# Kernel tuning notes

Measured on AMD Instinct MI355X. Metric: run time of the kernel, lower is better.

## Reference

```python
import jax, jax.numpy as jnp
import numpy as np

N_HEAD = 16
N_EMBD = 1024
HEAD_DIM = N_EMBD // N_HEAD


def setup_inputs() -> dict:
    key = jax.random.key(0)
    k1, k2, k3 = jax.random.split(key, 3)
    B, T, C = 4, 2048, N_EMBD
    scale = 1.0 / np.sqrt(C)
    x = jax.random.normal(k1, (B, T, C), dtype=jnp.float32)
    W_attn = jax.random.normal(k2, (C, 3 * C), dtype=jnp.float32) * scale
    W_proj = jax.random.normal(k3, (C, C), dtype=jnp.float32) * scale
    return {"x": x, "W_attn": W_attn, "W_proj": W_proj}


def reference(x, W_attn, W_proj):
    B, T, C = x.shape
    H, D = N_HEAD, HEAD_DIM
    qkv = x @ W_attn  # [B,T,3C]
    q, k, v = jnp.split(qkv, 3, axis=-1)
    # [B,H,T,D]
    q = q.reshape(B, T, H, D).transpose(0, 2, 1, 3)
    k = k.reshape(B, T, H, D).transpose(0, 2, 1, 3)
    v = v.reshape(B, T, H, D).transpose(0, 2, 1, 3)
    att = jnp.einsum("bhqd,bhkd->bhqk", q, k) * (1.0 / np.sqrt(D))
    mask = jnp.tril(jnp.ones((T, T), dtype=bool))
    att = jnp.where(mask, att, -jnp.inf)
    att = jax.nn.softmax(att, axis=-1)
    y = jnp.einsum("bhqk,bhkd->bhqd", att, v)
    y = y.transpose(0, 2, 1, 3).reshape(B, T, C)
    return y @ W_proj
```

## Files before the change

### kernel.cpp

```cpp
#include <hip/hip_runtime.h>
#include <hip/hip_bf16.h>

typedef __bf16 bf16x8 __attribute__((ext_vector_type(8)));
typedef __bf16 bf16x4 __attribute__((ext_vector_type(4)));
typedef float  f32x4  __attribute__((ext_vector_type(4)));

#define MFMA16(A, B, C) __builtin_amdgcn_mfma_f32_16x16x32_bf16((A), (B), (C), 0, 0, 0)

static constexpr int TB = 4;
static constexpr int TT = 2048;
static constexpr int TC = 1024;
static constexpr int TH = 16;
static constexpr int TD = 64;
static constexpr int TM = TB * TT;

__device__ __forceinline__ void gload16(const __bf16* g, __bf16* l) {
  __builtin_amdgcn_global_load_lds(
      (const __attribute__((address_space(1))) unsigned int*)g,
      (__attribute__((address_space(3))) unsigned int*)l, 16, 0, 0);
}

__device__ __forceinline__ void transpose_tile(const float* __restrict__ w,
                                               __bf16* __restrict__ wt,
                                               int K, int N, int bx, int by,
                                               __bf16 (*tile)[72], int tid) {
  const int k0 = by * 64, n0 = bx * 64;
#pragma unroll
  for (int it = 0; it < 4; ++it) {
    int c = tid + it * 256;
    int row = c >> 4, cc = (c & 15) * 4;
    float4 v = *(const float4*)(w + (size_t)(k0 + row) * N + n0 + cc);
    tile[row][cc + 0] = (__bf16)v.x;
    tile[row][cc + 1] = (__bf16)v.y;
    tile[row][cc + 2] = (__bf16)v.z;
    tile[row][cc + 3] = (__bf16)v.w;
  }
  __syncthreads();
#pragma unroll
  for (int it = 0; it < 2; ++it) {
    int c = tid + it * 256;
    int n = c >> 3, kk = (c & 7) * 8;
    bf16x8 v;
#pragma unroll
    for (int j = 0; j < 8; ++j) v[j] = tile[kk + j][n];
    *(bf16x8*)(wt + (size_t)(n0 + n) * K + k0 + kk) = v;
  }
}

__global__ __launch_bounds__(256) void k_prep(const float* __restrict__ x,
                                              __bf16* __restrict__ xb,
                                              const float* __restrict__ Wa,
                                              __bf16* __restrict__ wat,
                                              const float* __restrict__ Wp,
                                              __bf16* __restrict__ wpt) {
  __shared__ __align__(16) __bf16 tile[64][72];
  const int bid = blockIdx.x, tid = threadIdx.x;
  if (bid < 2048) {
    const int n4 = (TM * TC) / 4;
    const int stride = 2048 * 256;
    for (int i = bid * 256 + tid; i < n4; i += stride) {
      float4 v = *(const float4*)(x + (size_t)i * 4);
      bf16x4 o;
      o[0] = (__bf16)v.x; o[1] = (__bf16)v.y; o[2] = (__bf16)v.z; o[3] = (__bf16)v.w;
      *(bf16x4*)(xb + (size_t)i * 4) = o;
    }
  } else if (bid < 2816) {
    const int b2 = bid - 2048;
    transpose_tile(Wa, wat, 1024, 3072, b2 % 48, b2 / 48, tile, tid);
  } else {
    const int b2 = bid - 2816;
    transpose_tile(Wp, wpt, 1024, 1024, b2 % 16, b2 / 16, tile, tid);
  }
}

template <int EPI>
__global__ __launch_bounds__(256, 3) void k_gemm(const __bf16* __restrict__ A,
                                                 const __bf16* __restrict__ Bt,
                                                 int N, float* __restrict__ outf,
                                                 __bf16* __restrict__ Qo,
                                                 __bf16* __restrict__ Ko,
                                                 __bf16* __restrict__ Vto) {
  __shared__ __align__(16) __bf16 As[128 * 64];
  __shared__ __align__(16) __bf16 Bs[128 * 64];
  const int gx = gridDim.x;
  const int nwg = gx * gridDim.y;
  int id = blockIdx.y * gx + blockIdx.x;
  id = (id & 7) * (nwg >> 3) + (id >> 3);
  const int bm = id / gx, bn = id % gx;
  const int tid = threadIdx.x, lane = tid & 63, wid = tid >> 6;
  const int wr = wid >> 1, wc = wid & 1;
  const int lr = lane & 15, lg = lane >> 4;

  f32x4 acc[4][4];
  const f32x4 zero = {0.f, 0.f, 0.f, 0.f};
#pragma unroll
  for (int mi = 0; mi < 4; ++mi)
#pragma unroll
    for (int ni = 0; ni < 4; ++ni) acc[mi][ni] = zero;

  const __bf16* Ab = A + (size_t)bm * 128 * 1024;
  const __bf16* Bb = Bt + (size_t)bn * 128 * 1024;

  const int rr = wid * 8 + (lane >> 3);
  const int sc = (lane & 7) ^ (lane >> 3);

  int offA[4][2], offB[4][2];
#pragma unroll
  for (int i = 0; i < 4; ++i)
#pragma unroll
    for (int kk = 0; kk < 2; ++kk) {
      const int xo = ((((kk << 2) + lg) ^ (lr & 7)) << 3);
      offA[i][kk] = (wr * 64 + i * 16 + lr) * 64 + xo;
      offB[i][kk] = (wc * 64 + i * 16 + lr) * 64 + xo;
    }

  for (int k0 = 0; k0 < 1024; k0 += 64) {
#pragma unroll
    for (int it = 0; it < 4; ++it) {
      const int r = it * 32 + rr;
      gload16(Ab + (size_t)r * 1024 + k0 + sc * 8, As + it * 2048 + wid * 512);
      gload16(Bb + (size_t)r * 1024 + k0 + sc * 8, Bs + it * 2048 + wid * 512);
    }
    __syncthreads();

    bf16x8 af[4][2], bfr[4][2];
#pragma unroll
    for (int mi = 0; mi < 4; ++mi)
#pragma unroll
      for (int kk = 0; kk < 2; ++kk) {
        af[mi][kk]  = *(const bf16x8*)&As[offA[mi][kk]];
        bfr[mi][kk] = *(const bf16x8*)&Bs[offB[mi][kk]];
      }
#pragma unroll
    for (int mi = 0; mi < 4; ++mi)
#pragma unroll
      for (int ni = 0; ni < 4; ++ni) {
        acc[mi][ni] = MFMA16(af[mi][0], bfr[ni][0], acc[mi][ni]);
        acc[mi][ni] = MFMA16(af[mi][1], bfr[ni][1], acc[mi][ni]);
      }
    __syncthreads();
  }

  const int rb = bm * 128 + wr * 64 + lg * 4;
  const int cb = bn * 128 + wc * 64 + lr;
  if constexpr (EPI == 0) {
#pragma unroll
    for (int mi = 0; mi < 4; ++mi)
#pragma unroll
      for (int ni = 0; ni < 4; ++ni)
#pragma unroll
        for (int j = 0; j < 4; ++j)
          outf[(size_t)(rb + mi * 16 + j) * N + cb + ni * 16] = acc[mi][ni][j];
  } else {
    const int which = (bn * 128) >> 10;
    if (which == 2) {
#pragma unroll
      for (int mi = 0; mi < 4; ++mi) {
        const int r0 = rb + mi * 16;
        const int b = r0 >> 11, t0 = r0 & 2047;
#pragma unroll
        for (int ni = 0; ni < 4; ++ni) {
          const int c = cb + ni * 16;
          const int h = (c & 1023) >> 6, d = c & 63;
          bf16x4 pk;
#pragma unroll
          for (int j = 0; j < 4; ++j) pk[j] = (__bf16)acc[mi][ni][j];
          *(bf16x4*)(Vto + (((size_t)(b * TH + h) * TD + d) * TT) + t0) = pk;
        }
      }
    } else {
#pragma unroll
      for (int mi = 0; mi < 4; ++mi) {
#pragma unroll
        for (int ni = 0; ni < 4; ++ni) {
#pragma unroll
          for (int j = 0; j < 4; ++j) {
            float v = acc[mi][ni][j];
            int r = rb + mi * 16 + j;
            int c = cb + ni * 16;
            int within = c & 1023;
            int h = within >> 6, d = within & 63;
            int b = r >> 11, t = r & 2047;
            size_t idx = (((size_t)(b * TH + h)) * TT + t) * TD + d;
            if (which == 0)
              Qo[idx] = (__bf16)(v * 0.18033688f);
            else
              Ko[idx] = (__bf16)v;
          }
        }
      }
    }
  }
}

__global__ __launch_bounds__(256, 3) void k_attn(const __bf16* __restrict__ Qg,
                                                 const __bf16* __restrict__ Kg,
                                                 const __bf16* __restrict__ Vt,
                                                 __bf16* __restrict__ Y) {
  __shared__ __align__(16) __bf16 Ksh[2][64 * 64];
  __shared__ __align__(16) __bf16 Vsh[2][64 * 64];
  __shared__ __align__(16) __bf16 Plds[4][16][64];
  const int flat = blockIdx.x + (blockIdx.y << 4);
  const int W = (flat & 7) * 128 + (flat >> 3);
  const int bh = W >> 4, p = W & 15;
  const int tid = threadIdx.x, lane = tid & 63, w = tid >> 6;
  const int lr = lane & 15, lg = lane >> 4, lg8 = lg << 3, lg4 = lg << 2;

  const __bf16* Qb = Qg + ((size_t)bh * TT) * TD;
  const __bf16* Kb = Kg + ((size_t)bh * TT) * TD;
  const __bf16* Vb = Vt + ((size_t)bh * TD) * TT;
  const int b = bh >> 4, hh = bh & 15;
  __bf16* Yb = Y + ((size_t)b * TT) * TC + hh * TD;

  const int c0 = p, c1 = 31 - p;
  const int nkt0 = c0 + 1;
  const int nt = nkt0 + c1 + 1;

  const f32x4 zero = {0.f, 0.f, 0.f, 0.f};

  auto STAGE = [&](int bb, int kb) {
#pragma unroll
    for (int it = 0; it < 2; ++it) {
      int slot = tid + (it << 8);
      int r = slot >> 3;
      int sc = (slot & 7) ^ (r & 7);
      gload16(Kb + (size_t)(kb + r) * TD + sc * 8, &Ksh[bb][(it << 11) + (w << 9)]);
      gload16(Vb + (size_t)r * TT + kb + sc * 8, &Vsh[bb][(it << 11) + (w << 9)]);
    }
  };

  int off[4][2];
#pragma unroll
  for (int i = 0; i < 4; ++i)
#pragma unroll
    for (int h = 0; h < 2; ++h)
      off[i][h] = (i * 16 + lr) * 64 + ((((h << 2) + lg) ^ (lr & 7)) << 3);

  int wOff[4];
#pragma unroll
  for (int kf = 0; kf < 4; ++kf)
    wOff[kf] = ((((kf << 1) + (lg >> 1)) ^ (lr & 7)) << 3) + ((lg & 1) << 2);
  const int rOff0 = (lg ^ (lr & 7)) << 3;
  const int rOff1 = ((4 + lg) ^ (lr & 7)) << 3;

  int qw = c0 * 64 + w * 16;
  bf16x8 qf[2];
#pragma unroll
  for (int h = 0; h < 2; ++h)
    qf[h] = *(const bf16x8*)(Qb + (size_t)(qw + lr) * TD + h * 32 + lg8);
  f32x4 o[4];
  f32x4 l4 = zero;
#pragma unroll
  for (int df = 0; df < 4; ++df) o[df] = zero;

  auto epilogue = [&]() {
    float L = (l4[0] + l4[1]) + (l4[2] + l4[3]);
    L += __shfl_xor(L, 16);
    L += __shfl_xor(L, 32);
    const float inv = 1.0f / L;
#pragma unroll
    for (int j = 0; j < 4; ++j) {
      const float invr = __shfl(inv, lg4 + j);
      const int row = qw + lg4 + j;
#pragma unroll
      for (int df = 0; df < 4; ++df)
        Yb[(size_t)row * TC + df * 16 + lr] = (__bf16)(o[df][j] * invr);
    }
  };

  int cur = 0;
  STAGE(0, 0);
  __syncthreads();

  for (int t = 0; t < nt; ++t) {
    if (t + 1 < nt) {
      int t2 = t + 1;
      int kb2 = (t2 < nkt0 ? t2 : t2 - nkt0) << 6;
      STAGE(cur ^ 1, kb2);
    }
    if (t == nkt0) {
      epilogue();
      qw = c1 * 64 + w * 16;
#pragma unroll
      for (int h = 0; h < 2; ++h)
        qf[h] = *(const bf16x8*)(Qb + (size_t)(qw + lr) * TD + h * 32 + lg8);
      l4 = zero;
#pragma unroll
      for (int df = 0; df < 4; ++df) o[df] = zero;
    }

    const int kb = (t < nkt0 ? t : t - nkt0) << 6;
    const __bf16* Kt = Ksh[cur];
    const __bf16* Vst = Vsh[cur];

    bf16x8 kA[4][2];
#pragma unroll
    for (int kf = 0; kf < 4; ++kf)
#pragma unroll
      for (int h = 0; h < 2; ++h)
        kA[kf][h] = *(const bf16x8*)&Kt[off[kf][h]];

    f32x4 s4[4];
    __builtin_amdgcn_s_setprio(1);
#pragma unroll
    for (int kf = 0; kf < 4; ++kf) {
      f32x4 z = zero;
      z = MFMA16(kA[kf][0], qf[0], z);
      z = MFMA16(kA[kf][1], qf[1], z);
      s4[kf] = z;
    }
    __builtin_amdgcn_s_setprio(0);

    bf16x8 vB[4][2];
#pragma unroll
    for (int df = 0; df < 4; ++df)
#pragma unroll
      for (int h = 0; h < 2; ++h)
        vB[df][h] = *(const bf16x8*)&Vst[off[df][h]];

    {
      const int q = qw + lr;
      const bool diag = (kb + 63 > qw);
#pragma unroll
      for (int kf = 0; kf < 4; ++kf) {
#pragma unroll
        for (int j = 0; j < 4; ++j) {
          float arg = s4[kf][j];
          if (diag) {
            int key = kb + kf * 16 + lg4 + j;
            if (key > q) arg = -16384.0f;
          }
          s4[kf][j] = __builtin_amdgcn_exp2f(arg);
        }
        l4 += s4[kf];
        bf16x4 pk;
#pragma unroll
        for (int j = 0; j < 4; ++j) pk[j] = (__bf16)s4[kf][j];
        *(bf16x4*)&Plds[w][lr][wOff[kf]] = pk;
      }
    }

    __builtin_amdgcn_s_setprio(1);
    {
      bf16x8 pa0 = *(const bf16x8*)&Plds[w][lr][rOff0];
      bf16x8 pa1 = *(const bf16x8*)&Plds[w][lr][rOff1];
#pragma unroll
      for (int df = 0; df < 4; ++df) {
        o[df] = MFMA16(pa0, vB[df][0], o[df]);
        o[df] = MFMA16(pa1, vB[df][1], o[df]);
      }
    }
    __builtin_amdgcn_s_setprio(0);

    __syncthreads();
    cur ^= 1;
  }

  epilogue();
}

extern "C" void kernel_launch(void* const* d_in, const int* in_sizes, int n_in,
                              void* d_out, int out_size, void* d_ws, size_t ws_size,
                              hipStream_t stream) {
  const float* x  = (const float*)d_in[0];
  const float* Wa = (const float*)d_in[1];
  const float* Wp = (const float*)d_in[2];
  float* out = (float*)d_out;

  char* ws = (char*)d_ws;
  size_t off = 0;
  auto alloc = [&](size_t bytes) { char* p = ws + off; off += bytes; return p; };
  __bf16* xb   = (__bf16*)alloc((size_t)TM * TC * 2);
  __bf16* wat  = (__bf16*)alloc((size_t)3 * TC * TC * 2);
  __bf16* wpt  = (__bf16*)alloc((size_t)TC * TC * 2);
  __bf16* Qb   = (__bf16*)alloc((size_t)TM * TC * 2);
  __bf16* Kb   = (__bf16*)alloc((size_t)TM * TC * 2);
  __bf16* Vtb  = (__bf16*)alloc((size_t)TM * TC * 2);
  __bf16* Yb   = xb;

  k_prep<<<3072, 256, 0, stream>>>(x, xb, Wa, wat, Wp, wpt);
  k_gemm<1><<<dim3(24, 64), 256, 0, stream>>>(xb, wat, 3072, nullptr, Qb, Kb, Vtb);
  k_attn<<<dim3(16, 64), 256, 0, stream>>>(Qb, Kb, Vtb, Yb);
  k_gemm<0><<<dim3(8, 64), 256, 0, stream>>>(Yb, wpt, 1024, out, nullptr, nullptr, nullptr);
}
```

Before: 160.2 us.

## Process two adjacent query tiles per block sharing each K/V tile

Each attention block now owns two adjacent 64-row query chunks and computes both against every staged K/V tile, instead of handling chunks p and 31-p sequentially with separate key sweeps. This reuses each K/V LDS tile and fragment load for two query tiles, reducing global and LDS traffic per unit of work. The grid is remapped to a flat 1024-block launch with XCD-aware head grouping and alternating chunk order to soften the now uneven per-block work. It doubles accumulator registers, which risks occupancy, and loses the balanced pairing of the previous scheme.

```diff
diff --git a/kernel.cpp b/kernel.cpp
--- a/kernel.cpp
+++ b/kernel.cpp
@@ -200,9 +200,12 @@
   __shared__ __align__(16) __bf16 Ksh[2][64 * 64];
   __shared__ __align__(16) __bf16 Vsh[2][64 * 64];
   __shared__ __align__(16) __bf16 Plds[4][16][64];
-  const int flat = blockIdx.x + (blockIdx.y << 4);
-  const int W = (flat & 7) * 128 + (flat >> 3);
-  const int bh = W >> 4, p = W & 15;
+  const int flat = blockIdx.x;
+  const int xcd = flat & 7, bhHi = (flat >> 3) & 7, v = flat >> 6;
+  const int bh = (bhHi << 3) | xcd;
+  const int i = (bhHi & 1) ? (15 - v) : v;
+  const int cA = 2 * i;
+  const int nt = 2 * i + 2;
   const int tid = threadIdx.x, lane = tid & 63, w = tid >> 6;
   const int lr = lane & 15, lg = lane >> 4, lg8 = lg << 3, lg4 = lg << 2;
 
@@ -211,10 +214,6 @@
   const __bf16* Vb = Vt + ((size_t)bh * TD) * TT;
   const int b = bh >> 4, hh = bh & 15;
   __bf16* Yb = Y + ((size_t)b * TT) * TC + hh * TD;
-
-  const int c0 = p, c1 = 31 - p;
-  const int nkt0 = c0 + 1;
-  const int nt = nkt0 + c1 + 1;
 
   const f32x4 zero = {0.f, 0.f, 0.f, 0.f};
 
@@ -231,10 +230,10 @@
 
   int off[4][2];
 #pragma unroll
-  for (int i = 0; i < 4; ++i)
+  for (int ii = 0; ii < 4; ++ii)
 #pragma unroll
     for (int h = 0; h < 2; ++h)
-      off[i][h] = (i * 16 + lr) * 64 + ((((h << 2) + lg) ^ (lr & 7)) << 3);
+      off[ii][h] = (ii * 16 + lr) * 64 + ((((h << 2) + lg) ^ (lr & 7)) << 3);
 
   int wOff[4];
 #pragma unroll
@@ -243,17 +242,20 @@
   const int rOff0 = (lg ^ (lr & 7)) << 3;
   const int rOff1 = ((4 + lg) ^ (lr & 7)) << 3;
 
-  int qw = c0 * 64 + w * 16;
-  bf16x8 qf[2];
-#pragma unroll
-  for (int h = 0; h < 2; ++h)
-    qf[h] = *(const bf16x8*)(Qb + (size_t)(qw + lr) * TD + h * 32 + lg8);
-  f32x4 o[4];
-  f32x4 l4 = zero;
-#pragma unroll
-  for (int df = 0; df < 4; ++df) o[df] = zero;
-
-  auto epilogue = [&]() {
+  const int qwA = cA * 64 + w * 16;
+  const int qwB = (cA + 1) * 64 + w * 16;
+  bf16x8 qfA[2], qfB[2];
+#pragma unroll
+  for (int h = 0; h < 2; ++h) {
+    qfA[h] = *(const bf16x8*)(Qb + (size_t)(qwA + lr) * TD + h * 32 + lg8);
+    qfB[h] = *(const bf16x8*)(Qb + (size_t)(qwB + lr) * TD + h * 32 + lg8);
+  }
+  f32x4 oA[4], oB[4];
+  f32x4 lA = zero, lB = zero;
+#pragma unroll
+  for (int df = 0; df < 4; ++df) { oA[df] = zero; oB[df] = zero; }
+
+  auto epilogue = [&](int qw, f32x4 (&o)[4], f32x4& l4) {
     float L = (l4[0] + l4[1]) + (l4[2] + l4[3]);
     L += __shfl_xor(L, 16);
     L += __shfl_xor(L, 32);
@@ -273,25 +275,12 @@
   __syncthreads();
 
   for (int t = 0; t < nt; ++t) {
-    if (t + 1 < nt) {
-      int t2 = t + 1;
-      int kb2 = (t2 < nkt0 ? t2 : t2 - nkt0) << 6;
-      STAGE(cur ^ 1, kb2);
-    }
-    if (t == nkt0) {
-      epilogue();
-      qw = c1 * 64 + w * 16;
-#pragma unroll
-      for (int h = 0; h < 2; ++h)
-        qf[h] = *(const bf16x8*)(Qb + (size_t)(qw + lr) * TD + h * 32 + lg8);
-      l4 = zero;
-#pragma unroll
-      for (int df = 0; df < 4; ++df) o[df] = zero;
-    }
-
-    const int kb = (t < nkt0 ? t : t - nkt0) << 6;
+    if (t + 1 < nt) STAGE(cur ^ 1, (t + 1) << 6);
+
+    const int kb = t << 6;
     const __bf16* Kt = Ksh[cur];
     const __bf16* Vst = Vsh[cur];
+    const bool actA = (t + 1 < nt);
 
     bf16x8 kA[4][2];
 #pragma unroll
@@ -300,54 +289,99 @@
       for (int h = 0; h < 2; ++h)
         kA[kf][h] = *(const bf16x8*)&Kt[off[kf][h]];
 
-    f32x4 s4[4];
+    f32x4 s4a[4], s4b[4];
     __builtin_amdgcn_s_setprio(1);
 #pragma unroll
     for (int kf = 0; kf < 4; ++kf) {
       f32x4 z = zero;
-      z = MFMA16(kA[kf][0], qf[0], z);
-      z = MFMA16(kA[kf][1], qf[1], z);
-      s4[kf] = z;
+      z = MFMA16(kA[kf][0], qfB[0], z);
+      z = MFMA16(kA[kf][1], qfB[1], z);
+      s4b[kf] = z;
+    }
+    if (actA) {
+#pragma unroll
+      for (int kf = 0; kf < 4; ++kf) {
+        f32x4 z = zero;
+        z = MFMA16(kA[kf][0], qfA[0], z);
+        z = MFMA16(kA[kf][1], qfA[1], z);
+        s4a[kf] = z;
+      }
     }
     __builtin_amdgcn_s_setprio(0);
 
-    bf16x8 vB[4][2];
-#pragma unroll
-    for (int df = 0; df < 4; ++df)
-#pragma unroll
-      for (int h = 0; h < 2; ++h)
-        vB[df][h] = *(const bf16x8*)&Vst[off[df][h]];
-
-    {
-      const int q = qw + lr;
-      const bool diag = (kb + 63 > qw);
+    if (actA) {
+      const int q = qwA + lr;
+      const bool diag = (kb + 63 > qwA);
 #pragma unroll
       for (int kf = 0; kf < 4; ++kf) {
 #pragma unroll
         for (int j = 0; j < 4; ++j) {
-          float arg = s4[kf][j];
+          float arg = s4a[kf][j];
           if (diag) {
             int key = kb + kf * 16 + lg4 + j;
             if (key > q) arg = -16384.0f;
           }
-          s4[kf][j] = __builtin_amdgcn_exp2f(arg);
+          s4a[kf][j] = __builtin_amdgcn_exp2f(arg);
         }
-        l4 += s4[kf];
+        lA += s4a[kf];
         bf16x4 pk;
 #pragma unroll
-        for (int j = 0; j < 4; ++j) pk[j] = (__bf16)s4[kf][j];
+        for (int j = 0; j < 4; ++j) pk[j] = (__bf16)s4a[kf][j];
         *(bf16x4*)&Plds[w][lr][wOff[kf]] = pk;
       }
     }
 
+    bf16x4 pB[4];
+    {
+      const int q = qwB + lr;
+      const bool diag = (kb + 63 > qwB);
+#pragma unroll
+      for (int kf = 0; kf < 4; ++kf) {
+#pragma unroll
+        for (int j = 0; j < 4; ++j) {
+          float arg = s4b[kf][j];
+          if (diag) {
+            int key = kb + kf * 16 + lg4 + j;
+            if (key > q) arg = -16384.0f;
+          }
+          s4b[kf][j] = __builtin_amdgcn_exp2f(arg);
+        }
+        lB += s4b[kf];
+#pragma unroll
+        for (int j = 0; j < 4; ++j) pB[kf][j] = (__bf16)s4b[kf][j];
+      }
+    }
+
+    bf16x8 vB[4][2];
+#pragma unroll
+    for (int df = 0; df < 4; ++df)
+#pragma unroll
+      for (int h = 0; h < 2; ++h)
+        vB[df][h] = *(const bf16x8*)&Vst[off[df][h]];
+
+    if (actA) {
+      __builtin_amdgcn_s_setprio(1);
+      bf16x8 pa0 = *(const bf16x8*)&Plds[w][lr][rOff0];
+      bf16x8 pa1 = *(const bf16x8*)&Plds[w][lr][rOff1];
+#pragma unroll
+      for (int df = 0; df < 4; ++df) {
+        oA[df] = MFMA16(pa0, vB[df][0], oA[df]);
+        oA[df] = MFMA16(pa1, vB[df][1], oA[df]);
+      }
+      __builtin_amdgcn_s_setprio(0);
+    }
+
+#pragma unroll
+    for (int kf = 0; kf < 4; ++kf)
+      *(bf16x4*)&Plds[w][lr][wOff[kf]] = pB[kf];
     __builtin_amdgcn_s_setprio(1);
     {
       bf16x8 pa0 = *(const bf16x8*)&Plds[w][lr][rOff0];
       bf16x8 pa1 = *(const bf16x8*)&Plds[w][lr][rOff1];
 #pragma unroll
       for (int df = 0; df < 4; ++df) {
-        o[df] = MFMA16(pa0, vB[df][0], o[df]);
-        o[df] = MFMA16(pa1, vB[df][1], o[df]);
+        oB[df] = MFMA16(pa0, vB[df][0], oB[df]);
+        oB[df] = MFMA16(pa1, vB[df][1], oB[df]);
       }
     }
     __builtin_amdgcn_s_setprio(0);
@@ -356,7 +390,8 @@
     cur ^= 1;
   }
 
-  epilogue();
+  epilogue(qwA, oA, lA);
+  epilogue(qwB, oB, lB);
 }
 
 extern "C" void kernel_launch(void* const* d_in, const int* in_sizes, int n_in,
@@ -380,6 +415,6 @@
 
   k_prep<<<3072, 256, 0, stream>>>(x, xb, Wa, wat, Wp, wpt);
   k_gemm<1><<<dim3(24, 64), 256, 0, stream>>>(xb, wat, 3072, nullptr, Qb, Kb, Vtb);
-  k_attn<<<dim3(16, 64), 256, 0, stream>>>(Qb, Kb, Vtb, Yb);
+  k_attn<<<1024, 256, 0, stream>>>(Qb, Kb, Vtb, Yb);
   k_gemm<0><<<dim3(8, 64), 256, 0, stream>>>(Yb, wpt, 1024, out, nullptr, nullptr, nullptr);
 }
```

After: 180.2 us. 1.12x slower.
